# Kernel optimization log

Hardware: AMD Instinct MI355X
Metric: run time of the kernel (lower is better)

## Reference

```python
import jax, jax.numpy as jnp
import numpy as np

D_MODEL = 1024
D_STATE = 16
BATCH = 4
SEQLEN = 4096


def setup_inputs() -> dict:
    key = jax.random.key(0)
    kx, kA, kB, kC = jax.random.split(key, 4)
    x = jax.random.normal(kx, (BATCH, SEQLEN, D_MODEL), dtype=jnp.float32)
    # Params per init_weights(): A ~ N(-0.5, 0.1), B ~ N(0, 0.1), C ~ N(0, 0.1), D = 0
    A = -0.5 + 0.1 * jax.random.normal(kA, (1, D_STATE), dtype=jnp.float32)
    B_in = 0.1 * jax.random.normal(kB, (D_MODEL, D_STATE), dtype=jnp.float32)
    C = 0.1 * jax.random.normal(kC, (D_STATE, D_MODEL), dtype=jnp.float32)
    D = jnp.zeros((D_MODEL,), dtype=jnp.float32)
    return {"x": x, "A": A, "B_in": B_in, "C": C, "D": D}


def reference(x, A, B_in, C, D):
    # x: [B, N, E]; A: [1, S]; B_in: [E, S]; C: [S, E]; D: [E]
    A_neg = -jnp.exp(A)                              # [1, S]
    Bx = jnp.einsum('bne,es->bns', x, B_in)          # [B, N, S] = x @ B
    delta = jax.nn.softplus(Bx)                      # softplus(u @ B)
    decay = jnp.exp(delta * A_neg)                   # [B, N, S]

    def step(h, inp):
        d_t, bx_t = inp                              # each [B, S]
        h = h * d_t + bx_t
        return h, h

    h0 = jnp.zeros((x.shape[0], A.shape[1]), dtype=x.dtype)
    # scan over time: inputs [N, B, S]
    _, hs = jax.lax.scan(step, h0, (decay.transpose(1, 0, 2), Bx.transpose(1, 0, 2)))
    # readout: y_t = h_t @ C + x_t * D  (dropout p=0.0 -> identity)
    y = jnp.einsum('nbs,se->bne', hs, C) + x * D
    return y
```

## Files before the change

### kernel.cpp

```cpp
#include <hip/hip_runtime.h>

#define NSEQ 4096
#define EDIM 1024

#define OFF_PBX 0u
#define OFF_HT  1048576u

__device__ __forceinline__ void fma4(float4& a, float xv, const float4& b) {
    a.x = fmaf(xv, b.x, a.x);
    a.y = fmaf(xv, b.y, a.y);
    a.z = fmaf(xv, b.z, a.z);
    a.w = fmaf(xv, b.w, a.w);
}

__global__ __launch_bounds__(256, 4) void k1_bx(const float* __restrict__ x,
                                                const float* __restrict__ Bin,
                                                float* __restrict__ ws) {
    __shared__ float smem[2 * 64 * 65];

    const int tid  = threadIdx.x;
    const int lane = tid & 63;
    const int wu   = __builtin_amdgcn_readfirstlane(tid) >> 6;
    const int q    = blockIdx.x & 3;
    const int r0   = (blockIdx.x >> 2) * 64;
    const int b    = r0 >> 12;
    const int n0   = r0 & 4095;
    const int eq   = q * 256;

    const float4* xf4 = (const float4*)x;
    const float4* Bf4 = (const float4*)Bin;

    float acc[16];
#pragma unroll
    for (int s = 0; s < 16; s++) acc[s] = 0.f;

    float4 pf[4];
#pragma unroll
    for (int k = 0; k < 4; k++) {
        int i = tid + 256 * k, row = i >> 4, cq = i & 15;
        pf[k] = xf4[(size_t)(r0 + row) * 256 + q * 64 + cq];
    }
    {
        float* stg = smem;
#pragma unroll
        for (int k = 0; k < 4; k++) {
            int i = tid + 256 * k, row = i >> 4, cq = i & 15;
            float* p = &stg[row * 65 + cq * 4];
            p[0] = pf[k].x; p[1] = pf[k].y; p[2] = pf[k].z; p[3] = pf[k].w;
        }
    }
    __syncthreads();

    for (int c = 0; c < 4; ++c) {
        if (c < 3) {
#pragma unroll
            for (int k = 0; k < 4; k++) {
                int i = tid + 256 * k, row = i >> 4, cq = i & 15;
                pf[k] = xf4[(size_t)(r0 + row) * 256 + q * 64 + (c + 1) * 16 + cq];
            }
        }

        const float* stg = &smem[(c & 1) * 4160];
#pragma unroll
        for (int j = 0; j < 16; ++j) {
            const int el = wu * 16 + j;
            const int e  = eq + c * 64 + el;
            const float4 b0 = Bf4[e * 4 + 0];
            const float4 b1 = Bf4[e * 4 + 1];
            const float4 b2 = Bf4[e * 4 + 2];
            const float4 b3 = Bf4[e * 4 + 3];
            const float xv = stg[lane * 65 + el];
            acc[0]  = fmaf(xv, b0.x, acc[0]);  acc[1]  = fmaf(xv, b0.y, acc[1]);
            acc[2]  = fmaf(xv, b0.z, acc[2]);  acc[3]  = fmaf(xv, b0.w, acc[3]);
            acc[4]  = fmaf(xv, b1.x, acc[4]);  acc[5]  = fmaf(xv, b1.y, acc[5]);
            acc[6]  = fmaf(xv, b1.z, acc[6]);  acc[7]  = fmaf(xv, b1.w, acc[7]);
            acc[8]  = fmaf(xv, b2.x, acc[8]);  acc[9]  = fmaf(xv, b2.y, acc[9]);
            acc[10] = fmaf(xv, b2.z, acc[10]); acc[11] = fmaf(xv, b2.w, acc[11]);
            acc[12] = fmaf(xv, b3.x, acc[12]); acc[13] = fmaf(xv, b3.y, acc[13]);
            acc[14] = fmaf(xv, b3.z, acc[14]); acc[15] = fmaf(xv, b3.w, acc[15]);
        }

        if (c < 3) {
            float* dst = &smem[((c + 1) & 1) * 4160];
#pragma unroll
            for (int k = 0; k < 4; k++) {
                int i = tid + 256 * k, row = i >> 4, cq = i & 15;
                float* p = &dst[row * 65 + cq * 4];
                p[0] = pf[k].x; p[1] = pf[k].y; p[2] = pf[k].z; p[3] = pf[k].w;
            }
        }
        __syncthreads();
    }

    {
        const int rb = (wu * 64 + lane) * 17;
#pragma unroll
        for (int s = 0; s < 16; s++) smem[rb + s] = acc[s];
    }
    __syncthreads();

#pragma unroll
    for (int p = 0; p < 4; p++) {
        const int o   = tid + 256 * p;
        const int s   = o >> 6;
        const int row = o & 63;
        const float v = smem[(0 * 64 + row) * 17 + s] + smem[(1 * 64 + row) * 17 + s] +
                        smem[(2 * 64 + row) * 17 + s] + smem[(3 * 64 + row) * 17 + s];
        ws[OFF_PBX + (size_t)q * 262144u + (size_t)(b * 16 + s) * NSEQ + n0 + row] = v;
    }
}

__global__ __launch_bounds__(256) void k2_scan(const float* __restrict__ A,
                                               float* __restrict__ ws) {
    __shared__ float sP[4], sH[4];
    const int tid   = threadIdx.x;
    const int lane  = tid & 63;
    const int w     = tid >> 6;
    const int chain = blockIdx.x;
    const int bb    = chain >> 4, ss = chain & 15;

    float bx[16], de[16];
    const float Ae = expf(A[ss]);
#pragma unroll
    for (int k = 0; k < 4; k++) {
        float4 v4 = make_float4(0.f, 0.f, 0.f, 0.f);
#pragma unroll
        for (int q = 0; q < 4; q++) {
            const float4* Pq = (const float4*)(ws + OFF_PBX + (size_t)q * 262144u +
                                               (size_t)chain * NSEQ);
            float4 a = Pq[tid * 4 + k];
            v4.x += a.x; v4.y += a.y; v4.z += a.z; v4.w += a.w;
        }
        float vv[4] = {v4.x, v4.y, v4.z, v4.w};
#pragma unroll
        for (int j = 0; j < 4; j++) {
            float v  = vv[j];
            float sp = fmaxf(v, 0.f) + log1pf(expf(-fabsf(v)));
            bx[k * 4 + j] = v;
            de[k * 4 + j] = expf(-Ae * sp);
        }
    }

    float P = 1.f, h = 0.f;
#pragma unroll
    for (int k = 0; k < 16; k++) { h = fmaf(h, de[k], bx[k]); P *= de[k]; }

    float Pi = P, hi = h;
#pragma unroll
    for (int off = 1; off < 64; off <<= 1) {
        float Pp = __shfl_up(Pi, off, 64);
        float hp = __shfl_up(hi, off, 64);
        if (lane >= off) { hi = fmaf(hp, Pi, hi); Pi *= Pp; }
    }

    if (lane == 63) { sP[w] = Pi; sH[w] = hi; }
    __syncthreads();

    float hw = 0.f;
    for (int qq = 0; qq < w; qq++) hw = fmaf(hw, sP[qq], sH[qq]);

    float Pe = __shfl_up(Pi, 1, 64);
    float he = __shfl_up(hi, 1, 64);
    if (lane == 0) { Pe = 1.f; he = 0.f; }
    float hr = fmaf(hw, Pe, he);

    float* htp = ws + OFF_HT + ((size_t)bb * NSEQ + tid * 16) * 16 + ss;
#pragma unroll
    for (int k = 0; k < 16; k++) {
        hr = fmaf(hr, de[k], bx[k]);
        htp[k * 16] = hr;
    }
}

__global__ __launch_bounds__(256) void k3_out(const float* __restrict__ x,
                                              const float* __restrict__ C,
                                              const float* __restrict__ D,
                                              const float* __restrict__ ws,
                                              float* __restrict__ out) {
    const int tid = threadIdx.x;
    const int blk = blockIdx.x;
    const int tc  = blk & 255;
    const int b   = blk >> 8;
    const int t0  = tc * 16;

    const float4* C4 = (const float4*)C;
    float4 creg[16];
#pragma unroll
    for (int s = 0; s < 16; s++) creg[s] = C4[s * 256 + tid];
    float4 dreg = ((const float4*)D)[tid];

    const bool needX = __any((dreg.x != 0.f) | (dreg.y != 0.f) |
                             (dreg.z != 0.f) | (dreg.w != 0.f));

    const float* hb = ws + OFF_HT + ((size_t)b * NSEQ + t0) * 16;

    const float4* x4 = (const float4*)x;
    float4* o4 = (float4*)out;
    const size_t rowbase = ((size_t)b * NSEQ + t0) * 256;

    if (needX) {
#pragma unroll 4
        for (int tt = 0; tt < 16; tt++) {
            float4 xv = x4[rowbase + tt * 256 + tid];
            float4 y;
            y.x = xv.x * dreg.x; y.y = xv.y * dreg.y;
            y.z = xv.z * dreg.z; y.w = xv.w * dreg.w;
#pragma unroll
            for (int s = 0; s < 16; s++) fma4(y, hb[tt * 16 + s], creg[s]);
            o4[rowbase + tt * 256 + tid] = y;
        }
    } else {
#pragma unroll 4
        for (int tt = 0; tt < 16; tt++) {
            float4 y = make_float4(0.f, 0.f, 0.f, 0.f);
#pragma unroll
            for (int s = 0; s < 16; s++) fma4(y, hb[tt * 16 + s], creg[s]);
            o4[rowbase + tt * 256 + tid] = y;
        }
    }
}

extern "C" void kernel_launch(void* const* d_in, const int* in_sizes, int n_in,
                              void* d_out, int out_size, void* d_ws, size_t ws_size,
                              hipStream_t stream) {
    const float* x   = (const float*)d_in[0];
    const float* A   = (const float*)d_in[1];
    const float* Bin = (const float*)d_in[2];
    const float* C   = (const float*)d_in[3];
    const float* D   = (const float*)d_in[4];
    float* out = (float*)d_out;
    float* ws  = (float*)d_ws;

    hipLaunchKernelGGL(k1_bx,   dim3(1024), dim3(256), 0, stream, x, Bin, ws);
    hipLaunchKernelGGL(k2_scan, dim3(64),   dim3(256), 0, stream, A, ws);
    hipLaunchKernelGGL(k3_out,  dim3(1024), dim3(256), 0, stream, x, C, D, ws, out);
}
```

Before: 140.0 us.

## Split scan into chunked block-local scans with carry fix-up in output kernel

The scan kernel now runs 1024 blocks, each doing a local scan over a 256-step chunk of one chain, instead of 64 blocks each walking a whole 4096-step chain. It writes local h, inclusive decay products and per-chunk summaries. The output kernel combines the previous chunk summaries serially to get the carry-in state, rebuilds h in shared memory and does the readout. The k1 shared staging also moves to padded float4 stores and loads. This trades a heavily underfilled scan launch for extra workspace traffic and redundant carry work in k3.

```diff
diff --git a/kernel.cpp b/kernel.cpp
--- a/kernel.cpp
+++ b/kernel.cpp
@@ -3,8 +3,10 @@
 #define NSEQ 4096
 #define EDIM 1024
 
-#define OFF_PBX 0u
-#define OFF_HT  1048576u
+#define OFF_PBX  0u
+#define OFF_HLOC 1048576u
+#define OFF_PINC 1310720u
+#define OFF_SUM  1572864u
 
 __device__ __forceinline__ void fma4(float4& a, float xv, const float4& b) {
     a.x = fmaf(xv, b.x, a.x);
@@ -16,8 +18,7 @@
 __global__ __launch_bounds__(256, 4) void k1_bx(const float* __restrict__ x,
                                                 const float* __restrict__ Bin,
                                                 float* __restrict__ ws) {
-    __shared__ float smem[2 * 64 * 65];
-
+    __shared__ __align__(16) float smem[2 * 64 * 68];
     const int tid  = threadIdx.x;
     const int lane = tid & 63;
     const int wu   = __builtin_amdgcn_readfirstlane(tid) >> 6;
@@ -40,14 +41,10 @@
         int i = tid + 256 * k, row = i >> 4, cq = i & 15;
         pf[k] = xf4[(size_t)(r0 + row) * 256 + q * 64 + cq];
     }
-    {
-        float* stg = smem;
-#pragma unroll
-        for (int k = 0; k < 4; k++) {
-            int i = tid + 256 * k, row = i >> 4, cq = i & 15;
-            float* p = &stg[row * 65 + cq * 4];
-            p[0] = pf[k].x; p[1] = pf[k].y; p[2] = pf[k].z; p[3] = pf[k].w;
-        }
+#pragma unroll
+    for (int k = 0; k < 4; k++) {
+        int i = tid + 256 * k, row = i >> 4, cq = i & 15;
+        *(float4*)&smem[row * 68 + cq * 4] = pf[k];
     }
     __syncthreads();
 
@@ -59,34 +56,35 @@
                 pf[k] = xf4[(size_t)(r0 + row) * 256 + q * 64 + (c + 1) * 16 + cq];
             }
         }
-
-        const float* stg = &smem[(c & 1) * 4160];
-#pragma unroll
-        for (int j = 0; j < 16; ++j) {
-            const int el = wu * 16 + j;
-            const int e  = eq + c * 64 + el;
-            const float4 b0 = Bf4[e * 4 + 0];
-            const float4 b1 = Bf4[e * 4 + 1];
-            const float4 b2 = Bf4[e * 4 + 2];
-            const float4 b3 = Bf4[e * 4 + 3];
-            const float xv = stg[lane * 65 + el];
-            acc[0]  = fmaf(xv, b0.x, acc[0]);  acc[1]  = fmaf(xv, b0.y, acc[1]);
-            acc[2]  = fmaf(xv, b0.z, acc[2]);  acc[3]  = fmaf(xv, b0.w, acc[3]);
-            acc[4]  = fmaf(xv, b1.x, acc[4]);  acc[5]  = fmaf(xv, b1.y, acc[5]);
-            acc[6]  = fmaf(xv, b1.z, acc[6]);  acc[7]  = fmaf(xv, b1.w, acc[7]);
-            acc[8]  = fmaf(xv, b2.x, acc[8]);  acc[9]  = fmaf(xv, b2.y, acc[9]);
-            acc[10] = fmaf(xv, b2.z, acc[10]); acc[11] = fmaf(xv, b2.w, acc[11]);
-            acc[12] = fmaf(xv, b3.x, acc[12]); acc[13] = fmaf(xv, b3.y, acc[13]);
-            acc[14] = fmaf(xv, b3.z, acc[14]); acc[15] = fmaf(xv, b3.w, acc[15]);
-        }
-
+        const float* stg = &smem[(c & 1) * 4352];
+#pragma unroll
+        for (int jj = 0; jj < 4; ++jj) {
+            const float4 xq = *(const float4*)&stg[lane * 68 + wu * 16 + jj * 4];
+            const float xs[4] = {xq.x, xq.y, xq.z, xq.w};
+#pragma unroll
+            for (int m = 0; m < 4; ++m) {
+                const int e = eq + c * 64 + wu * 16 + jj * 4 + m;
+                const float4 b0 = Bf4[e * 4 + 0];
+                const float4 b1 = Bf4[e * 4 + 1];
+                const float4 b2 = Bf4[e * 4 + 2];
+                const float4 b3 = Bf4[e * 4 + 3];
+                const float xv = xs[m];
+                acc[0]  = fmaf(xv, b0.x, acc[0]);  acc[1]  = fmaf(xv, b0.y, acc[1]);
+                acc[2]  = fmaf(xv, b0.z, acc[2]);  acc[3]  = fmaf(xv, b0.w, acc[3]);
+                acc[4]  = fmaf(xv, b1.x, acc[4]);  acc[5]  = fmaf(xv, b1.y, acc[5]);
+                acc[6]  = fmaf(xv, b1.z, acc[6]);  acc[7]  = fmaf(xv, b1.w, acc[7]);
+                acc[8]  = fmaf(xv, b2.x, acc[8]);  acc[9]  = fmaf(xv, b2.y, acc[9]);
+                acc[10] = fmaf(xv, b2.z, acc[10]); acc[11] = fmaf(xv, b2.w, acc[11]);
+                acc[12] = fmaf(xv, b3.x, acc[12]); acc[13] = fmaf(xv, b3.y, acc[13]);
+                acc[14] = fmaf(xv, b3.z, acc[14]); acc[15] = fmaf(xv, b3.w, acc[15]);
+            }
+        }
         if (c < 3) {
-            float* dst = &smem[((c + 1) & 1) * 4160];
+            float* dst = &smem[((c + 1) & 1) * 4352];
 #pragma unroll
             for (int k = 0; k < 4; k++) {
                 int i = tid + 256 * k, row = i >> 4, cq = i & 15;
-                float* p = &dst[row * 65 + cq * 4];
-                p[0] = pf[k].x; p[1] = pf[k].y; p[2] = pf[k].z; p[3] = pf[k].w;
+                *(float4*)&dst[row * 68 + cq * 4] = pf[k];
             }
         }
         __syncthreads();
@@ -116,59 +114,39 @@
     const int tid   = threadIdx.x;
     const int lane  = tid & 63;
     const int w     = tid >> 6;
-    const int chain = blockIdx.x;
-    const int bb    = chain >> 4, ss = chain & 15;
-
-    float bx[16], de[16];
+    const int chain = blockIdx.x >> 4;
+    const int chunk = blockIdx.x & 15;
+    const int ss    = chain & 15;
+    const int t     = chunk * 256 + tid;
+
+    float bxv = 0.f;
+#pragma unroll
+    for (int q = 0; q < 4; q++)
+        bxv += ws[OFF_PBX + (size_t)q * 262144u + (size_t)chain * NSEQ + t];
+
     const float Ae = expf(A[ss]);
-#pragma unroll
-    for (int k = 0; k < 4; k++) {
-        float4 v4 = make_float4(0.f, 0.f, 0.f, 0.f);
-#pragma unroll
-        for (int q = 0; q < 4; q++) {
-            const float4* Pq = (const float4*)(ws + OFF_PBX + (size_t)q * 262144u +
-                                               (size_t)chain * NSEQ);
-            float4 a = Pq[tid * 4 + k];
-            v4.x += a.x; v4.y += a.y; v4.z += a.z; v4.w += a.w;
-        }
-        float vv[4] = {v4.x, v4.y, v4.z, v4.w};
-#pragma unroll
-        for (int j = 0; j < 4; j++) {
-            float v  = vv[j];
-            float sp = fmaxf(v, 0.f) + log1pf(expf(-fabsf(v)));
-            bx[k * 4 + j] = v;
-            de[k * 4 + j] = expf(-Ae * sp);
-        }
-    }
-
-    float P = 1.f, h = 0.f;
-#pragma unroll
-    for (int k = 0; k < 16; k++) { h = fmaf(h, de[k], bx[k]); P *= de[k]; }
-
-    float Pi = P, hi = h;
+    const float sp = fmaxf(bxv, 0.f) + log1pf(expf(-fabsf(bxv)));
+    const float de = expf(-Ae * sp);
+
+    float Pi = de, hi = bxv;
 #pragma unroll
     for (int off = 1; off < 64; off <<= 1) {
         float Pp = __shfl_up(Pi, off, 64);
         float hp = __shfl_up(hi, off, 64);
         if (lane >= off) { hi = fmaf(hp, Pi, hi); Pi *= Pp; }
     }
-
     if (lane == 63) { sP[w] = Pi; sH[w] = hi; }
     __syncthreads();
-
-    float hw = 0.f;
-    for (int qq = 0; qq < w; qq++) hw = fmaf(hw, sP[qq], sH[qq]);
-
-    float Pe = __shfl_up(Pi, 1, 64);
-    float he = __shfl_up(hi, 1, 64);
-    if (lane == 0) { Pe = 1.f; he = 0.f; }
-    float hr = fmaf(hw, Pe, he);
-
-    float* htp = ws + OFF_HT + ((size_t)bb * NSEQ + tid * 16) * 16 + ss;
-#pragma unroll
-    for (int k = 0; k < 16; k++) {
-        hr = fmaf(hr, de[k], bx[k]);
-        htp[k * 16] = hr;
+    float Hw = 0.f, Pw = 1.f;
+    for (int qq = 0; qq < w; qq++) { Hw = fmaf(Hw, sP[qq], sH[qq]); Pw *= sP[qq]; }
+
+    const float hloc = fmaf(Hw, Pi, hi);
+    const float pinc = Pw * Pi;
+    ws[OFF_HLOC + (size_t)chain * NSEQ + t] = hloc;
+    ws[OFF_PINC + (size_t)chain * NSEQ + t] = pinc;
+    if (tid == 255) {
+        ws[OFF_SUM + (chain * 16 + chunk) * 2 + 0] = pinc;
+        ws[OFF_SUM + (chain * 16 + chunk) * 2 + 1] = hloc;
     }
 }
 
@@ -177,22 +155,38 @@
                                               const float* __restrict__ D,
                                               const float* __restrict__ ws,
                                               float* __restrict__ out) {
+    __shared__ float sh[16 * 17];
     const int tid = threadIdx.x;
     const int blk = blockIdx.x;
     const int tc  = blk & 255;
     const int b   = blk >> 8;
     const int t0  = tc * 16;
+    const int chunk = t0 >> 8;
+
+    {
+        const int s  = tid >> 4;
+        const int tt = tid & 15;
+        const int chain = b * 16 + s;
+        float H = 0.f;
+        for (int c = 0; c < chunk; ++c) {
+            const float Pc = ws[OFF_SUM + (chain * 16 + c) * 2 + 0];
+            const float hc = ws[OFF_SUM + (chain * 16 + c) * 2 + 1];
+            H = fmaf(H, Pc, hc);
+        }
+        const int t = t0 + tt;
+        const float h = fmaf(ws[OFF_PINC + (size_t)chain * NSEQ + t], H,
+                             ws[OFF_HLOC + (size_t)chain * NSEQ + t]);
+        sh[tt * 17 + s] = h;
+    }
 
     const float4* C4 = (const float4*)C;
     float4 creg[16];
 #pragma unroll
     for (int s = 0; s < 16; s++) creg[s] = C4[s * 256 + tid];
-    float4 dreg = ((const float4*)D)[tid];
-
+    const float4 dreg = ((const float4*)D)[tid];
     const bool needX = __any((dreg.x != 0.f) | (dreg.y != 0.f) |
                              (dreg.z != 0.f) | (dreg.w != 0.f));
-
-    const float* hb = ws + OFF_HT + ((size_t)b * NSEQ + t0) * 16;
+    __syncthreads();
 
     const float4* x4 = (const float4*)x;
     float4* o4 = (float4*)out;
@@ -206,7 +200,7 @@
             y.x = xv.x * dreg.x; y.y = xv.y * dreg.y;
             y.z = xv.z * dreg.z; y.w = xv.w * dreg.w;
 #pragma unroll
-            for (int s = 0; s < 16; s++) fma4(y, hb[tt * 16 + s], creg[s]);
+            for (int s = 0; s < 16; s++) fma4(y, sh[tt * 17 + s], creg[s]);
             o4[rowbase + tt * 256 + tid] = y;
         }
     } else {
@@ -214,7 +208,7 @@
         for (int tt = 0; tt < 16; tt++) {
             float4 y = make_float4(0.f, 0.f, 0.f, 0.f);
 #pragma unroll
-            for (int s = 0; s < 16; s++) fma4(y, hb[tt * 16 + s], creg[s]);
+            for (int s = 0; s < 16; s++) fma4(y, sh[tt * 17 + s], creg[s]);
             o4[rowbase + tt * 256 + tid] = y;
         }
     }
@@ -232,6 +226,6 @@
     float* ws  = (float*)d_ws;
 
     hipLaunchKernelGGL(k1_bx,   dim3(1024), dim3(256), 0, stream, x, Bin, ws);
-    hipLaunchKernelGGL(k2_scan, dim3(64),   dim3(256), 0, stream, A, ws);
+    hipLaunchKernelGGL(k2_scan, dim3(1024), dim3(256), 0, stream, A, ws);
     hipLaunchKernelGGL(k3_out,  dim3(1024), dim3(256), 0, stream, x, C, D, ws, out);
 }
```

After: 147.2 us. 1.05x slower.
